# Performance work log

Hardware: AMD Instinct MI355X
Metric: run time of the kernel (lower is better)

The kernel has to match this reference:

```python
import jax, jax.numpy as jnp
import numpy as np

B, N, IN, H, DK, DV, OUT = 8, 1024, 512, 8, 64, 64, 512
SCALE = 1.0 / (DK ** 0.5)


def setup_inputs() -> dict:
    key = jax.random.key(0)
    ks = jax.random.split(key, 10)
    s = lambda fan_in: 1.0 / np.sqrt(fan_in)
    return {
        "x": jax.random.normal(ks[0], (B, N, IN), dtype=jnp.float32),
        "Wv": jax.random.uniform(ks[1], (IN, H * DV), jnp.float32, -s(IN), s(IN)),
        "bv": jax.random.uniform(ks[2], (H * DV,), jnp.float32, -s(IN), s(IN)),
        "Wk": jax.random.uniform(ks[3], (IN, H * DK), jnp.float32, -s(IN), s(IN)),
        "bk": jax.random.uniform(ks[4], (H * DK,), jnp.float32, -s(IN), s(IN)),
        "Wq": jax.random.uniform(ks[5], (IN, H * DK), jnp.float32, -s(IN), s(IN)),
        "bq": jax.random.uniform(ks[6], (H * DK,), jnp.float32, -s(IN), s(IN)),
        "Wo": jax.random.uniform(ks[7], (H * DV, OUT), jnp.float32, -s(H * DV), s(H * DV)),
        "bo": jax.random.uniform(ks[8], (OUT,), jnp.float32, -s(H * DV), s(H * DV)),
        "mask": jax.random.randint(ks[9], (B, N, N), 0, 2, dtype=jnp.int32),
    }


def reference(x, Wv, bv, Wk, bk, Wq, bq, Wo, bo, mask):
    # projections -> (B, N, H, d), vkq activation = relu
    v = jax.nn.relu((x @ Wv + bv).reshape(B, N, H, DV))
    q = jax.nn.relu((x @ Wq + bq).reshape(B, N, H, DK))
    k = jax.nn.relu((x @ Wk + bk).reshape(B, N, H, DK))
    # (B, H, N, d)
    q, k, v = (t.transpose(0, 2, 1, 3) for t in (q, k, v))
    # raw attention weights (returned pre-mask, pre-softmax): (B, H, N, N)
    att_weights = jnp.einsum("bhqd,bhkd->bhqk", q, k) * SCALE
    att = jnp.where(mask[:, None, :, :] == 0, -1e9, att_weights)
    att = jax.nn.softmax(att, axis=-1)
    out = jnp.einsum("bhqk,bhkd->bhqd", att, v) + v  # residual add of v
    out = out.transpose(0, 2, 1, 3).reshape(B, N, H * DV)
    out = jax.nn.relu(out @ Wo + bo)  # final activation = relu
    return out, att_weights
```

## Files before the change

### kernel.cpp

```cpp
#include <hip/hip_runtime.h>
#include <hip/hip_bf16.h>

typedef __attribute__((ext_vector_type(8))) short short8;
typedef __attribute__((ext_vector_type(4))) float f32x4;

#define DEV static __device__ __forceinline__

DEV unsigned short f2bf(float f) {
  union { float f; unsigned u; } v; v.f = f;
  unsigned r = v.u + 0x7FFFu + ((v.u >> 16) & 1u);
  return (unsigned short)(r >> 16);
}
DEV float bf2f(unsigned short b) {
  union { unsigned u; float f; } v; v.u = ((unsigned)b) << 16;
  return v.f;
}

DEV unsigned cvtpk_bf16(float lo, float hi) {
  unsigned r;
  asm("v_cvt_pk_bf16_f32 %0, %1, %2" : "=v"(r) : "v"(lo), "v"(hi));
  return r;
}

DEV void gld_lds16(const void* g, void* l) {
  __builtin_amdgcn_global_load_lds(
      (const __attribute__((address_space(1))) unsigned int*)g,
      (__attribute__((address_space(3))) unsigned int*)l, 16, 0, 0);
}

DEV short8 lds_read8(const unsigned short* base, int byteoff) {
  return *reinterpret_cast<const short8*>(reinterpret_cast<const char*>(base) + byteoff);
}

__global__ __launch_bounds__(256) void prep_kernel(
    const float* __restrict__ x, unsigned short* __restrict__ xb,
    const float* __restrict__ W0, const float* __restrict__ W1,
    const float* __restrict__ W2, const float* __restrict__ W3,
    unsigned short* __restrict__ T0, unsigned short* __restrict__ T1,
    unsigned short* __restrict__ T2, unsigned short* __restrict__ T3,
    const int* __restrict__ mask, unsigned char* __restrict__ mb) {
  __shared__ unsigned short tile[32][33];
  const int bid = blockIdx.x, tid = threadIdx.x;
  if (bid < 4096) {
    int i = bid * 256 + tid;
    float4 v = reinterpret_cast<const float4*>(x)[i];
    ushort4 o;
    o.x = f2bf(v.x); o.y = f2bf(v.y); o.z = f2bf(v.z); o.w = f2bf(v.w);
    reinterpret_cast<ushort4*>(xb)[i] = o;
  } else if (bid < 5120) {
    int r = bid - 4096;
    int z = r >> 8;
    r &= 255;
    const float* W = z == 0 ? W0 : z == 1 ? W1 : z == 2 ? W2 : W3;
    unsigned short* T = z == 0 ? T0 : z == 1 ? T1 : z == 2 ? T2 : T3;
    int tx = tid & 31, ty = tid >> 5;
    int n0 = (r & 15) * 32, k0 = (r >> 4) * 32;
#pragma unroll
    for (int i = 0; i < 32; i += 8)
      tile[ty + i][tx] = f2bf(W[(size_t)(k0 + ty + i) * 512 + n0 + tx]);
    __syncthreads();
#pragma unroll
    for (int i = 0; i < 32; i += 8)
      T[(size_t)(n0 + ty + i) * 512 + k0 + tx] = tile[tx][ty + i];
  } else {
    int i = (bid - 5120) * 256 + tid;
    int4 m4 = reinterpret_cast<const int4*>(mask)[i];
    unsigned v = (m4.x ? 1u : 0u) | ((m4.y ? 1u : 0u) << 8) |
                 ((m4.z ? 1u : 0u) << 16) | ((m4.w ? 1u : 0u) << 24);
    reinterpret_cast<unsigned*>(mb)[i] = v;
  }
}

__global__ __launch_bounds__(256) void mask_prep_kernel(const int* __restrict__ mask,
                                                        unsigned char* __restrict__ mb) {
  int i = blockIdx.x * 256 + threadIdx.x;
  int4 m4 = reinterpret_cast<const int4*>(mask)[i];
  unsigned v = (m4.x ? 1u : 0u) | ((m4.y ? 1u : 0u) << 8) |
               ((m4.z ? 1u : 0u) << 16) | ((m4.w ? 1u : 0u) << 24);
  reinterpret_cast<unsigned*>(mb)[i] = v;
}

__global__ __launch_bounds__(256) void gemm_proj_kernel(
    const unsigned short* __restrict__ xb,
    const unsigned short* __restrict__ WqT, const unsigned short* __restrict__ WkT,
    const unsigned short* __restrict__ WvT,
    const float* __restrict__ bq, const float* __restrict__ bk, const float* __restrict__ bv,
    unsigned short* __restrict__ qn, unsigned short* __restrict__ kn,
    unsigned short* __restrict__ vn, unsigned short* __restrict__ vT) {
  const int z = blockIdx.z;
  const unsigned short* Wt = z == 0 ? WqT : z == 1 ? WkT : WvT;
  const float* bias = z == 0 ? bq : z == 1 ? bk : bv;
  unsigned short* outp = z == 0 ? qn : z == 1 ? kn : vn;

  __shared__ unsigned short smem[17408];
  unsigned short* As = smem;
  unsigned short* Bs = smem + 4096;

  const int tid = threadIdx.x;
  const int lane = tid & 63;
  const int w = tid >> 6;
  const int wm = w >> 1, wn = w & 1;
  const int lr = lane & 15;
  const int g = lane >> 4;

  const int m0 = blockIdx.x * 128;
  const int n0 = blockIdx.y * 128;

  f32x4 acc[4][4];
#pragma unroll
  for (int i = 0; i < 4; ++i)
#pragma unroll
    for (int j = 0; j < 4; ++j) acc[i][j] = (f32x4){0.f, 0.f, 0.f, 0.f};

  for (int kt = 0; kt < 16; ++kt) {
    const int k0 = kt * 32;
    __syncthreads();
#pragma unroll
    for (int p = 0; p < 2; ++p) {
      int slot = tid + 256 * p;
      int r = slot >> 2;
      int kg = (slot & 3) ^ ((r >> 1) & 3);
      unsigned short* ldsA = As + (size_t)((tid >> 6) + 4 * p) * 512;
      unsigned short* ldsB = Bs + (size_t)((tid >> 6) + 4 * p) * 512;
      gld_lds16(xb + (size_t)(m0 + r) * 512 + k0 + kg * 8, ldsA);
      gld_lds16(Wt + (size_t)(n0 + r) * 512 + k0 + kg * 8, ldsB);
    }
    __syncthreads();
    short8 af[4], bfr[4];
#pragma unroll
    for (int mi = 0; mi < 4; ++mi) {
      int r = wm * 64 + mi * 16 + lr;
      af[mi] = lds_read8(As, (r * 64 + g * 16) ^ (((r >> 1) & 3) << 4));
    }
#pragma unroll
    for (int ni = 0; ni < 4; ++ni) {
      int r = wn * 64 + ni * 16 + lr;
      bfr[ni] = lds_read8(Bs, (r * 64 + g * 16) ^ (((r >> 1) & 3) << 4));
    }
#pragma unroll
    for (int mi = 0; mi < 4; ++mi)
#pragma unroll
      for (int ni = 0; ni < 4; ++ni)
        acc[mi][ni] = __builtin_amdgcn_mfma_f32_16x16x32_bf16(af[mi], bfr[ni], acc[mi][ni], 0, 0, 0);
  }
  __syncthreads();

  float biasv[4];
#pragma unroll
  for (int ni = 0; ni < 4; ++ni) biasv[ni] = bias[n0 + wn * 64 + ni * 16 + lr];

#pragma unroll
  for (int mi = 0; mi < 4; ++mi) {
    int rowb = m0 + wm * 64 + mi * 16 + g * 4;
#pragma unroll
    for (int ni = 0; ni < 4; ++ni) {
      int c = n0 + wn * 64 + ni * 16 + lr;
      int h = c >> 6, d = c & 63;
#pragma unroll
      for (int rr = 0; rr < 4; ++rr) {
        float vf = acc[mi][ni][rr] + biasv[ni];
        vf = vf > 0.f ? vf : 0.f;
        unsigned short bvv = f2bf(vf);
        int row = rowb + rr;
        int b = row >> 10, tok = row & 1023;
        outp[((size_t)(b * 8 + h) * 1024 + tok) * 64 + d] = bvv;
        if (z == 2) {
          int cl = wn * 64 + ni * 16 + lr;
          int rl = wm * 64 + mi * 16 + g * 4 + rr;
          smem[cl * 136 + rl] = bvv;
        }
      }
    }
  }
  if (z == 2) {
    __syncthreads();
    int cl = tid >> 1, half = tid & 1;
    int gc = n0 + cl, h = gc >> 6, d = gc & 63;
    int b = m0 >> 10;
    int tokbase = (m0 & 1023) + half * 64;
    size_t base = (size_t)(b * 8 + h) * 65536 + (size_t)d * 1024 + tokbase;
    const unsigned short* src = smem + cl * 136 + half * 64;
#pragma unroll
    for (int j = 0; j < 8; ++j) {
      short8 v8 = *reinterpret_cast<const short8*>(src + j * 8);
      *reinterpret_cast<short8*>(vT + base + j * 8) = v8;
    }
  }
}

__global__ __launch_bounds__(512) void attn_kernel(
    const unsigned short* __restrict__ qg, const unsigned short* __restrict__ kgp,
    const unsigned short* __restrict__ vg, const unsigned short* __restrict__ vTg,
    const unsigned char* __restrict__ mb, float* __restrict__ attw,
    unsigned short* __restrict__ Og) {
  __shared__ unsigned short Ks[2][4096];
  __shared__ unsigned short Vs[2][4096];
  __shared__ unsigned short Ps[8192];

  const int tid = threadIdx.x, lane = tid & 63, w = tid >> 6;
  const int lr = lane & 15, g = lane >> 4;

  const int bid = blockIdx.x;
  const int b = bid & 7;
  const int idx = bid >> 3;
  const int h = idx >> 3;
  const int qc = idx & 7;
  const int bh = b * 8 + h;

  const int qw = qc * 128 + w * 16;
  const size_t qbase = (size_t)bh * 65536;

  const unsigned short* kbase = kgp + qbase;
  const unsigned short* vbase = vTg + qbase;

  const int srow = w * 8 + (lane >> 3);
  const int ssw = ((lane & 7) ^ (srow & 7)) * 8;

  short8 aq[2];
#pragma unroll
  for (int dc = 0; dc < 2; ++dc)
    aq[dc] = *reinterpret_cast<const short8*>(
        qg + qbase + (size_t)(qw + lr) * 64 + dc * 32 + g * 8);

  f32x4 o[4];
#pragma unroll
  for (int di = 0; di < 4; ++di) o[di] = (f32x4){0.f, 0.f, 0.f, 0.f};
  float lsum = 0.f;

  unsigned short* Pw = Ps + w * 1024;
  const unsigned char* mp = mb + ((size_t)(b * 1024 + qw + lr)) * 1024 + g * 4;
  float* awp = attw + ((size_t)bh * 1024 + qw + lr) * 1024 + g * 4;

  gld_lds16(kbase + (size_t)srow * 64 + ssw, reinterpret_cast<char*>(Ks[0]) + w * 1024);
  gld_lds16(vbase + (size_t)srow * 1024 + ssw, reinterpret_cast<char*>(Vs[0]) + w * 1024);
  asm volatile("s_waitcnt vmcnt(0)" ::: "memory");
  __builtin_amdgcn_sched_barrier(0);
  __builtin_amdgcn_s_barrier();

  int cur = 0;
  for (int t = 0; t < 16; ++t) {
    const int kv0 = t * 64;

    unsigned mk[4];
#pragma unroll
    for (int ni = 0; ni < 4; ++ni)
      mk[ni] = *reinterpret_cast<const unsigned*>(mp + kv0 + ni * 16);
    __builtin_amdgcn_sched_barrier(0);

    if (t < 15) {
      const int kn0 = kv0 + 64;
      gld_lds16(kbase + (size_t)(kn0 + srow) * 64 + ssw,
                reinterpret_cast<char*>(Ks[cur ^ 1]) + w * 1024);
      gld_lds16(vbase + (size_t)srow * 1024 + kn0 + ssw,
                reinterpret_cast<char*>(Vs[cur ^ 1]) + w * 1024);
    }
    __builtin_amdgcn_sched_barrier(0);

    const unsigned short* Kc = Ks[cur];
    const unsigned short* Vc = Vs[cur];

    f32x4 s[4];
    __builtin_amdgcn_s_setprio(1);
#pragma unroll
    for (int ni = 0; ni < 4; ++ni) {
      int row = ni * 16 + lr;
      s[ni] = (f32x4){0.f, 0.f, 0.f, 0.f};
#pragma unroll
      for (int dc = 0; dc < 2; ++dc) {
        short8 ak = lds_read8(Kc, (row * 128 + dc * 64 + g * 16) ^ ((row & 7) << 4));
        s[ni] = __builtin_amdgcn_mfma_f32_16x16x32_bf16(ak, aq[dc], s[ni], 0, 0, 0);
      }
    }
    __builtin_amdgcn_s_setprio(0);

#pragma unroll
    for (int ni = 0; ni < 4; ++ni) {
      f32x4 sv = s[ni] * 0.125f;
      *reinterpret_cast<f32x4*>(awp + kv0 + ni * 16) = sv;
      unsigned m = mk[ni];
      float p0 = (m & 0x000000FFu) ? __expf(sv[0] - 16.f) : 0.f;
      float p1 = (m & 0x0000FF00u) ? __expf(sv[1] - 16.f) : 0.f;
      float p2 = (m & 0x00FF0000u) ? __expf(sv[2] - 16.f) : 0.f;
      float p3 = (m & 0xFF000000u) ? __expf(sv[3] - 16.f) : 0.f;
      lsum += (p0 + p1) + (p2 + p3);
      uint2 pk = make_uint2(cvtpk_bf16(p0, p1), cvtpk_bf16(p2, p3));
      int pbyte = (lr * 128 + ni * 32 + g * 8) ^ ((lr & 7) << 4);
      *reinterpret_cast<uint2*>(reinterpret_cast<char*>(Pw) + pbyte) = pk;
    }

    __builtin_amdgcn_s_setprio(1);
#pragma unroll
    for (int kc = 0; kc < 2; ++kc) {
      short8 ap = lds_read8(Pw, (lr * 128 + kc * 64 + g * 16) ^ ((lr & 7) << 4));
#pragma unroll
      for (int di = 0; di < 4; ++di) {
        int rd = di * 16 + lr;
        short8 bv8 = lds_read8(Vc, (rd * 128 + kc * 64 + g * 16) ^ ((rd & 7) << 4));
        o[di] = __builtin_amdgcn_mfma_f32_16x16x32_bf16(ap, bv8, o[di], 0, 0, 0);
      }
    }
    __builtin_amdgcn_s_setprio(0);

    asm volatile("s_waitcnt vmcnt(4)" ::: "memory");
    __builtin_amdgcn_sched_barrier(0);
    __builtin_amdgcn_s_barrier();
    __builtin_amdgcn_sched_barrier(0);
    cur ^= 1;
  }

  float l = lsum;
  l += __shfl_xor(l, 16);
  l += __shfl_xor(l, 32);

#pragma unroll
  for (int rr = 0; rr < 4; ++rr) {
    int gq2 = qw + g * 4 + rr;
    float lq = __shfl(l, g * 4 + rr);
    float inv = 1.f / lq;
#pragma unroll
    for (int di = 0; di < 4; ++di) {
      int gd = di * 16 + lr;
      float ov = o[di][rr] * inv + bf2f(vg[qbase + (size_t)gq2 * 64 + gd]);
      Og[((size_t)(b * 1024 + gq2)) * 512 + h * 64 + gd] = f2bf(ov);
    }
  }
}

__global__ __launch_bounds__(256) void gemm_out_kernel(
    const unsigned short* __restrict__ Ab, const unsigned short* __restrict__ WoT,
    const float* __restrict__ bo, float* __restrict__ outp) {
  __shared__ unsigned short smem[8192];
  unsigned short* As = smem;
  unsigned short* Bs = smem + 4096;

  const int tid = threadIdx.x;
  const int lane = tid & 63;
  const int w = tid >> 6;
  const int wm = w >> 1, wn = w & 1;
  const int lr = lane & 15;
  const int g = lane >> 4;
  const int m0 = blockIdx.x * 128;
  const int n0 = blockIdx.y * 128;

  f32x4 acc[4][4];
#pragma unroll
  for (int i = 0; i < 4; ++i)
#pragma unroll
    for (int j = 0; j < 4; ++j) acc[i][j] = (f32x4){0.f, 0.f, 0.f, 0.f};

  for (int kt = 0; kt < 16; ++kt) {
    const int k0 = kt * 32;
    __syncthreads();
#pragma unroll
    for (int p = 0; p < 2; ++p) {
      int slot = tid + 256 * p;
      int r = slot >> 2;
      int kg = (slot & 3) ^ ((r >> 1) & 3);
      unsigned short* ldsA = As + (size_t)((tid >> 6) + 4 * p) * 512;
      unsigned short* ldsB = Bs + (size_t)((tid >> 6) + 4 * p) * 512;
      gld_lds16(Ab + (size_t)(m0 + r) * 512 + k0 + kg * 8, ldsA);
      gld_lds16(WoT + (size_t)(n0 + r) * 512 + k0 + kg * 8, ldsB);
    }
    __syncthreads();
    short8 af[4], bfr[4];
#pragma unroll
    for (int mi = 0; mi < 4; ++mi) {
      int r = wm * 64 + mi * 16 + lr;
      af[mi] = lds_read8(As, (r * 64 + g * 16) ^ (((r >> 1) & 3) << 4));
    }
#pragma unroll
    for (int ni = 0; ni < 4; ++ni) {
      int r = wn * 64 + ni * 16 + lr;
      bfr[ni] = lds_read8(Bs, (r * 64 + g * 16) ^ (((r >> 1) & 3) << 4));
    }
#pragma unroll
    for (int mi = 0; mi < 4; ++mi)
#pragma unroll
      for (int ni = 0; ni < 4; ++ni)
        acc[mi][ni] = __builtin_amdgcn_mfma_f32_16x16x32_bf16(af[mi], bfr[ni], acc[mi][ni], 0, 0, 0);
  }

  float biasv[4];
#pragma unroll
  for (int ni = 0; ni < 4; ++ni) biasv[ni] = bo[n0 + wn * 64 + ni * 16 + lr];
#pragma unroll
  for (int mi = 0; mi < 4; ++mi) {
    int rowb = m0 + wm * 64 + mi * 16 + g * 4;
#pragma unroll
    for (int ni = 0; ni < 4; ++ni) {
      int c = n0 + wn * 64 + ni * 16 + lr;
#pragma unroll
      for (int rr = 0; rr < 4; ++rr) {
        float vf = acc[mi][ni][rr] + biasv[ni];
        outp[(size_t)(rowb + rr) * 512 + c] = vf > 0.f ? vf : 0.f;
      }
    }
  }
}

extern "C" void kernel_launch(void* const* d_in, const int* in_sizes, int n_in,
                              void* d_out, int out_size, void* d_ws, size_t ws_size,
                              hipStream_t stream) {
  const float* x = (const float*)d_in[0];
  const float* Wv = (const float*)d_in[1];
  const float* bv = (const float*)d_in[2];
  const float* Wk = (const float*)d_in[3];
  const float* bk = (const float*)d_in[4];
  const float* Wq = (const float*)d_in[5];
  const float* bq = (const float*)d_in[6];
  const float* Wo = (const float*)d_in[7];
  const float* bo = (const float*)d_in[8];
  const int* mask = (const int*)d_in[9];

  char* ws = (char*)d_ws;
  unsigned short* xb  = (unsigned short*)(ws);
  unsigned short* WqT = (unsigned short*)(ws + 8388608);
  unsigned short* WkT = (unsigned short*)(ws + 8912896);
  unsigned short* WvT = (unsigned short*)(ws + 9437184);
  unsigned short* WoT = (unsigned short*)(ws + 9961472);
  unsigned short* qn  = (unsigned short*)(ws + 10485760);
  unsigned short* kn  = (unsigned short*)(ws + 18874368);
  unsigned short* vn  = (unsigned short*)(ws + 27262976);
  unsigned short* vT  = (unsigned short*)(ws + 35651584);
  unsigned short* Og  = (unsigned short*)(ws + 44040192);

  const size_t MBB_HI = 52428800;
  const bool big = ws_size >= MBB_HI + 8388608;
  unsigned char* mbb = big ? (unsigned char*)(ws + MBB_HI) : (unsigned char*)ws;

  float* outp = (float*)d_out;
  float* attw = (float*)d_out + 4194304;

  prep_kernel<<<big ? 13312 : 5120, 256, 0, stream>>>(
      x, xb, Wq, Wk, Wv, Wo, WqT, WkT, WvT, WoT, mask, mbb);

  dim3 gp(64, 4, 3);
  gemm_proj_kernel<<<gp, 256, 0, stream>>>(xb, WqT, WkT, WvT, bq, bk, bv, qn, kn, vn, vT);

  if (!big) mask_prep_kernel<<<8192, 256, 0, stream>>>(mask, mbb);

  attn_kernel<<<512, 512, 0, stream>>>(qn, kn, vn, vT, mbb, attw, Og);

  dim3 go(64, 4);
  gemm_out_kernel<<<go, 256, 0, stream>>>(Og, WoT, bo, outp);
}
```

Before: 132.6 us.

## Double-buffer LDS tiles in projection and output GEMMs to overlap loads with MFMA

Both GEMM kernels now use two LDS buffers. The next K-tile is staged asynchronously while MFMAs run on the current one, and the second barrier per iteration is removed. Wave priority is raised around the MFMA block. The goal is to hide global-to-LDS latency, at the cost of doubled LDS use in gemm_out, which may reduce occupancy.

```diff
diff --git a/kernel.cpp b/kernel.cpp
--- a/kernel.cpp
+++ b/kernel.cpp
@@ -94,7 +94,7 @@
 
   __shared__ unsigned short smem[17408];
   unsigned short* As = smem;
-  unsigned short* Bs = smem + 4096;
+  unsigned short* Bs = smem + 8192;
 
   const int tid = threadIdx.x;
   const int lane = tid & 63;
@@ -112,38 +112,56 @@
 #pragma unroll
     for (int j = 0; j < 4; ++j) acc[i][j] = (f32x4){0.f, 0.f, 0.f, 0.f};
 
+#define STAGE_AB(buf, k0)                                                         \
+  {                                                                               \
+    _Pragma("unroll") for (int p = 0; p < 2; ++p) {                               \
+      int slot = tid + 256 * p;                                                   \
+      int r = slot >> 2;                                                          \
+      int kg = (slot & 3) ^ ((r >> 1) & 3);                                       \
+      unsigned short* ldsA = As + (buf)*4096 + (size_t)(w + 4 * p) * 512;         \
+      unsigned short* ldsB = Bs + (buf)*4096 + (size_t)(w + 4 * p) * 512;         \
+      gld_lds16(xb + (size_t)(m0 + r) * 512 + (k0) + kg * 8, ldsA);               \
+      gld_lds16(Wt + (size_t)(n0 + r) * 512 + (k0) + kg * 8, ldsB);               \
+    }                                                                             \
+  }
+
+  STAGE_AB(0, 0)
+  asm volatile("s_waitcnt vmcnt(0)" ::: "memory");
+  __builtin_amdgcn_sched_barrier(0);
+  __builtin_amdgcn_s_barrier();
+
+  int cur = 0;
   for (int kt = 0; kt < 16; ++kt) {
-    const int k0 = kt * 32;
-    __syncthreads();
-#pragma unroll
-    for (int p = 0; p < 2; ++p) {
-      int slot = tid + 256 * p;
-      int r = slot >> 2;
-      int kg = (slot & 3) ^ ((r >> 1) & 3);
-      unsigned short* ldsA = As + (size_t)((tid >> 6) + 4 * p) * 512;
-      unsigned short* ldsB = Bs + (size_t)((tid >> 6) + 4 * p) * 512;
-      gld_lds16(xb + (size_t)(m0 + r) * 512 + k0 + kg * 8, ldsA);
-      gld_lds16(Wt + (size_t)(n0 + r) * 512 + k0 + kg * 8, ldsB);
-    }
-    __syncthreads();
+    if (kt < 15) STAGE_AB(cur ^ 1, (kt + 1) * 32)
+    __builtin_amdgcn_sched_barrier(0);
+
+    const unsigned short* Ac = As + cur * 4096;
+    const unsigned short* Bc = Bs + cur * 4096;
     short8 af[4], bfr[4];
 #pragma unroll
     for (int mi = 0; mi < 4; ++mi) {
       int r = wm * 64 + mi * 16 + lr;
-      af[mi] = lds_read8(As, (r * 64 + g * 16) ^ (((r >> 1) & 3) << 4));
+      af[mi] = lds_read8(Ac, (r * 64 + g * 16) ^ (((r >> 1) & 3) << 4));
     }
 #pragma unroll
     for (int ni = 0; ni < 4; ++ni) {
       int r = wn * 64 + ni * 16 + lr;
-      bfr[ni] = lds_read8(Bs, (r * 64 + g * 16) ^ (((r >> 1) & 3) << 4));
-    }
+      bfr[ni] = lds_read8(Bc, (r * 64 + g * 16) ^ (((r >> 1) & 3) << 4));
+    }
+    __builtin_amdgcn_s_setprio(1);
 #pragma unroll
     for (int mi = 0; mi < 4; ++mi)
 #pragma unroll
       for (int ni = 0; ni < 4; ++ni)
         acc[mi][ni] = __builtin_amdgcn_mfma_f32_16x16x32_bf16(af[mi], bfr[ni], acc[mi][ni], 0, 0, 0);
-  }
-  __syncthreads();
+    __builtin_amdgcn_s_setprio(0);
+
+    asm volatile("s_waitcnt vmcnt(0)" ::: "memory");
+    __builtin_amdgcn_sched_barrier(0);
+    __builtin_amdgcn_s_barrier();
+    __builtin_amdgcn_sched_barrier(0);
+    cur ^= 1;
+  }
 
   float biasv[4];
 #pragma unroll
@@ -186,6 +204,7 @@
       *reinterpret_cast<short8*>(vT + base + j * 8) = v8;
     }
   }
+#undef STAGE_AB
 }
 
 __global__ __launch_bounds__(512) void attn_kernel(
@@ -329,9 +348,9 @@
 __global__ __launch_bounds__(256) void gemm_out_kernel(
     const unsigned short* __restrict__ Ab, const unsigned short* __restrict__ WoT,
     const float* __restrict__ bo, float* __restrict__ outp) {
-  __shared__ unsigned short smem[8192];
+  __shared__ unsigned short smem[16384];
   unsigned short* As = smem;
-  unsigned short* Bs = smem + 4096;
+  unsigned short* Bs = smem + 8192;
 
   const int tid = threadIdx.x;
   const int lane = tid & 63;
@@ -348,37 +367,57 @@
 #pragma unroll
     for (int j = 0; j < 4; ++j) acc[i][j] = (f32x4){0.f, 0.f, 0.f, 0.f};
 
+#define STAGE_AB(buf, k0)                                                         \
+  {                                                                               \
+    _Pragma("unroll") for (int p = 0; p < 2; ++p) {                               \
+      int slot = tid + 256 * p;                                                   \
+      int r = slot >> 2;                                                          \
+      int kg = (slot & 3) ^ ((r >> 1) & 3);                                       \
+      unsigned short* ldsA = As + (buf)*4096 + (size_t)(w + 4 * p) * 512;         \
+      unsigned short* ldsB = Bs + (buf)*4096 + (size_t)(w + 4 * p) * 512;         \
+      gld_lds16(Ab + (size_t)(m0 + r) * 512 + (k0) + kg * 8, ldsA);               \
+      gld_lds16(WoT + (size_t)(n0 + r) * 512 + (k0) + kg * 8, ldsB);              \
+    }                                                                             \
+  }
+
+  STAGE_AB(0, 0)
+  asm volatile("s_waitcnt vmcnt(0)" ::: "memory");
+  __builtin_amdgcn_sched_barrier(0);
+  __builtin_amdgcn_s_barrier();
+
+  int cur = 0;
   for (int kt = 0; kt < 16; ++kt) {
-    const int k0 = kt * 32;
-    __syncthreads();
-#pragma unroll
-    for (int p = 0; p < 2; ++p) {
-      int slot = tid + 256 * p;
-      int r = slot >> 2;
-      int kg = (slot & 3) ^ ((r >> 1) & 3);
-      unsigned short* ldsA = As + (size_t)((tid >> 6) + 4 * p) * 512;
-      unsigned short* ldsB = Bs + (size_t)((tid >> 6) + 4 * p) * 512;
-      gld_lds16(Ab + (size_t)(m0 + r) * 512 + k0 + kg * 8, ldsA);
-      gld_lds16(WoT + (size_t)(n0 + r) * 512 + k0 + kg * 8, ldsB);
-    }
-    __syncthreads();
+    if (kt < 15) STAGE_AB(cur ^ 1, (kt + 1) * 32)
+    __builtin_amdgcn_sched_barrier(0);
+
+    const unsigned short* Ac = As + cur * 4096;
+    const unsigned short* Bc = Bs + cur * 4096;
     short8 af[4], bfr[4];
 #pragma unroll
     for (int mi = 0; mi < 4; ++mi) {
       int r = wm * 64 + mi * 16 + lr;
-      af[mi] = lds_read8(As, (r * 64 + g * 16) ^ (((r >> 1) & 3) << 4));
+      af[mi] = lds_read8(Ac, (r * 64 + g * 16) ^ (((r >> 1) & 3) << 4));
     }
 #pragma unroll
     for (int ni = 0; ni < 4; ++ni) {
       int r = wn * 64 + ni * 16 + lr;
-      bfr[ni] = lds_read8(Bs, (r * 64 + g * 16) ^ (((r >> 1) & 3) << 4));
-    }
+      bfr[ni] = lds_read8(Bc, (r * 64 + g * 16) ^ (((r >> 1) & 3) << 4));
+    }
+    __builtin_amdgcn_s_setprio(1);
 #pragma unroll
     for (int mi = 0; mi < 4; ++mi)
 #pragma unroll
       for (int ni = 0; ni < 4; ++ni)
         acc[mi][ni] = __builtin_amdgcn_mfma_f32_16x16x32_bf16(af[mi], bfr[ni], acc[mi][ni], 0, 0, 0);
-  }
+    __builtin_amdgcn_s_setprio(0);
+
+    asm volatile("s_waitcnt vmcnt(0)" ::: "memory");
+    __builtin_amdgcn_sched_barrier(0);
+    __builtin_amdgcn_s_barrier();
+    __builtin_amdgcn_sched_barrier(0);
+    cur ^= 1;
+  }
+#undef STAGE_AB
 
   float biasv[4];
 #pragma unroll
```

New measurement: 132.4 us, median of 3. About the same (-0.2%).
